# Optimization experiments

Hardware: AMD Instinct MI355X
Metric: run time of the kernel (lower is better)

The kernel has to match this reference:

```python
import jax, jax.numpy as jnp
import numpy as np

B, T, NH, HS = 2, 2048, 16, 64
C = NH * HS
V_SHIFT = 1          # value shift; queries start at position V_SHIFT
EXP_SCALE = 10.0     # exp_param_scale
KB_UP = 5.0          # kernel_beta_upbound


def setup_inputs() -> dict:
    key = jax.random.key(0)
    ks = jax.random.split(key, 8)
    s = 0.02
    return {
        "x": jax.random.normal(ks[0], (B, T, C), jnp.float32),
        # leaky-average key path: linear proj + per-head decay coefficient
        "W_la": jax.random.normal(ks[1], (C, C), jnp.float32) * s,
        "la_coef": jax.random.uniform(ks[2], (NH,), jnp.float32, 0.1, 0.9),
        "kernel_beta": jnp.ones((NH,), jnp.float32) / EXP_SCALE,
        "value_beta": jnp.ones((NH,), jnp.float32) * (-0.5) / EXP_SCALE,
        # value featurizer (lowrlinearconv): linear + per-head mixing coef
        "W_v": jax.random.normal(ks[3], (C, C), jnp.float32) * s,
        "v_coef": jax.random.uniform(ks[4], (NH,), jnp.float32, 0.0, 1.0),
        "W_proj": jax.random.normal(ks[5], (C, C), jnp.float32) * s,
    }


def reference(x, W_la, la_coef, kernel_beta, value_beta, W_v, v_coef, W_proj):
    B_, T_, C_ = x.shape
    # ---- keys: leaky average (per-head EMA recurrence) of linear projection ----
    xl = (x @ W_la).reshape(B_, T_, NH, HS)          # (B,T,nh,hs)
    alpha = la_coef.reshape(NH, 1)                   # per-head decay

    def step(carry, xt):  # carry,xt: (B,nh,hs)
        new = alpha * carry + (1.0 - alpha) * xt
        return new, new

    _, kt = jax.lax.scan(step, jnp.zeros((B_, NH, HS), x.dtype),
                         jnp.swapaxes(xl, 0, 1))    # (T,B,nh,hs)
    k = jnp.transpose(kt, (1, 2, 0, 3))              # (B,nh,T,hs)
    k = k / jnp.linalg.norm(k, axis=-1, keepdims=True)
    kb = jnp.exp(jnp.minimum(kernel_beta * EXP_SCALE, KB_UP)).reshape(1, NH, 1, 1)
    k = k * kb

    # ---- values: lowrlinearconv featurizer (shift=1, kernel=2) + L2 norm ----
    xv = (x @ W_v).reshape(B_, T_, NH, HS).transpose(0, 2, 1, 3)   # (B,nh,T,hs)
    xv_sh = jnp.concatenate([xv[:, :, 1:], jnp.zeros_like(xv[:, :, :1])], axis=2)
    c = v_coef.reshape(1, NH, 1, 1)
    v = xv_sh * (1.0 - c) + xv * c
    v = v / jnp.linalg.norm(v, axis=-1, keepdims=True)
    v = v * jnp.exp(value_beta * EXP_SCALE).reshape(1, NH, 1, 1)

    # ---- shifted-causal masked SDPA (scale=1); queries are positions >= V_SHIFT ----
    q = k[:, :, V_SHIFT:]                            # (B,nh,T-1,hs)
    scores = jnp.einsum('bhqd,bhkd->bhqk', q, k)
    qpos = jnp.arange(V_SHIFT, T_)[:, None]
    kpos = jnp.arange(T_)[None, :]
    mask = kpos < qpos                               # key j visible iff j < query position
    scores = jnp.where(mask, scores, -jnp.inf)
    att = jax.nn.softmax(scores, axis=-1)
    y_att = jnp.einsum('bhqk,bhkd->bhqd', att, v)
    y = jnp.concatenate([jnp.zeros((B_, NH, V_SHIFT, HS), x.dtype), y_att], axis=2)
    y = jnp.transpose(y, (0, 2, 1, 3)).reshape(B_, T_, C_)
    return y @ W_proj                                # dropouts are eval-mode identity
```

## Files before the change

kernel.cpp:

```cpp
#include <hip/hip_runtime.h>
#include <hip/hip_bf16.h>

#define B_  2
#define T_  2048
#define NH_ 16
#define HS_ 64
#define C_  1024
#define SCL_ 128
#define SCN_ (T_ / SCL_)
#define NT_  (T_ / 64)
#define TEL_ 4096

typedef __attribute__((ext_vector_type(8))) short bf16x8;
typedef __attribute__((ext_vector_type(4))) float f32x4;

__device__ inline int pack_bf16(float a, float b) {
  union { __hip_bfloat16 h; unsigned short u; } ua, ub;
  ua.h = __float2bfloat16(a);
  ub.h = __float2bfloat16(b);
  return (int)(((unsigned)ub.u << 16) | (unsigned)ua.u);
}

__device__ inline void gl_lds16(const __hip_bfloat16* g, __hip_bfloat16* l) {
  __builtin_amdgcn_global_load_lds(
      (const __attribute__((address_space(1))) unsigned int*)g,
      (__attribute__((address_space(3))) unsigned int*)l, 16, 0, 0);
}

__global__ __launch_bounds__(256) void cvt_bf16_kernel(const float* __restrict__ in,
                                                       __hip_bfloat16* __restrict__ out) {
  const int i = (blockIdx.x * 256 + threadIdx.x) * 8;
  const float4 a = *reinterpret_cast<const float4*>(in + i);
  const float4 b = *reinterpret_cast<const float4*>(in + i + 4);
  union { int s[4]; int4 v; } u;
  u.s[0] = pack_bf16(a.x, a.y);
  u.s[1] = pack_bf16(a.z, a.w);
  u.s[2] = pack_bf16(b.x, b.y);
  u.s[3] = pack_bf16(b.z, b.w);
  *reinterpret_cast<int4*>(out + i) = u.v;
}

__global__ __launch_bounds__(256) void cvtT_all_kernel(const float* __restrict__ W_la,
                                                       const float* __restrict__ W_v,
                                                       const float* __restrict__ W_proj,
                                                       __hip_bfloat16* __restrict__ Wcat,
                                                       __hip_bfloat16* __restrict__ WprojT) {
  __shared__ __hip_bfloat16 tile[64][66];
  const int z = blockIdx.z;
  const float* W = (z == 0) ? W_la : (z == 1) ? W_v : W_proj;
  __hip_bfloat16* WT = (z == 2) ? WprojT : Wcat + (size_t)z * C_ * C_;
  const int w = threadIdx.x >> 6, l = threadIdx.x & 63;
  const int n0 = blockIdx.x * 64, k0 = blockIdx.y * 64;
#pragma unroll
  for (int r = 0; r < 16; ++r) {
    const int k = k0 + w * 16 + r;
    tile[w * 16 + r][l] = __float2bfloat16(W[(size_t)k * C_ + n0 + l]);
  }
  __syncthreads();
#pragma unroll
  for (int r = 0; r < 16; ++r) {
    const int nn = w * 16 + r;
    WT[(size_t)(n0 + nn) * C_ + k0 + l] = tile[l][nn];
  }
}

__global__ __launch_bounds__(256) void gemm_in_kernel(const __hip_bfloat16* __restrict__ A,
                                                      const __hip_bfloat16* __restrict__ BT,
                                                      float* __restrict__ C0,
                                                      float* __restrict__ C1) {
  __shared__ __hip_bfloat16 As[2 * 128 * 32];
  __shared__ __hip_bfloat16 Bs[2 * 128 * 32];
  const int tid = threadIdx.x;
  const int m0 = blockIdx.y * 128, n0 = blockIdx.x * 128;
  const int w = tid >> 6, l = tid & 63;
  const int n = l & 15, kg = l >> 4;
  const int m0w = (w & 1) * 64, n0w = (w >> 1) * 64;

  const int r0 = tid >> 2, o0 = (tid & 3) * 8;
  const __hip_bfloat16* ag0 = A + (size_t)(m0 + r0) * C_ + o0;
  const __hip_bfloat16* ag1 = A + (size_t)(m0 + 64 + r0) * C_ + o0;
  const __hip_bfloat16* bg0 = BT + (size_t)(n0 + r0) * C_ + o0;
  const __hip_bfloat16* bg1 = BT + (size_t)(n0 + 64 + r0) * C_ + o0;

  f32x4 acc[4][4];
#pragma unroll
  for (int i = 0; i < 4; ++i)
#pragma unroll
    for (int j = 0; j < 4; ++j) acc[i][j] = f32x4{0.f, 0.f, 0.f, 0.f};

  auto stage = [&](int kk, int buf) {
    __hip_bfloat16* a = As + buf * 4096;
    __hip_bfloat16* b = Bs + buf * 4096;
    gl_lds16(ag0 + kk, a + tid * 8);
    gl_lds16(ag1 + kk, a + 2048 + tid * 8);
    gl_lds16(bg0 + kk, b + tid * 8);
    gl_lds16(bg1 + kk, b + 2048 + tid * 8);
  };

  stage(0, 0);
  int cur = 0;
  for (int k0 = 0; k0 < C_; k0 += 32) {
    asm volatile("" ::: "memory");
    __builtin_amdgcn_s_barrier();
    asm volatile("" ::: "memory");
    if (k0 + 32 < C_) {
      stage(k0 + 32, cur ^ 1);
      asm volatile("s_waitcnt vmcnt(4)" ::: "memory");
    } else {
      asm volatile("s_waitcnt vmcnt(0)" ::: "memory");
    }
    __builtin_amdgcn_s_barrier();
    asm volatile("" ::: "memory");

    const __hip_bfloat16* Ab = As + cur * 4096;
    const __hip_bfloat16* Bb = Bs + cur * 4096;
    bf16x8 af[4], bf[4];
#pragma unroll
    for (int ms = 0; ms < 4; ++ms)
      af[ms] = *reinterpret_cast<const bf16x8*>(Ab + (m0w + ms * 16 + n) * 32 + kg * 8);
#pragma unroll
    for (int ns = 0; ns < 4; ++ns)
      bf[ns] = *reinterpret_cast<const bf16x8*>(Bb + (n0w + ns * 16 + n) * 32 + kg * 8);
#pragma unroll
    for (int ms = 0; ms < 4; ++ms)
#pragma unroll
      for (int ns = 0; ns < 4; ++ns)
        acc[ms][ns] = __builtin_amdgcn_mfma_f32_16x16x32_bf16(af[ms], bf[ns], acc[ms][ns], 0, 0, 0);
    cur ^= 1;
  }

  float* Cb = (n0 < C_) ? C0 : C1;
  const int nc = (n0 < C_) ? n0 : n0 - C_;
#pragma unroll
  for (int ms = 0; ms < 4; ++ms) {
#pragma unroll
    for (int r = 0; r < 4; ++r) {
      const int row = m0 + m0w + ms * 16 + kg * 4 + r;
      float* cp = Cb + (size_t)row * C_ + nc + n0w + n;
#pragma unroll
      for (int ns = 0; ns < 4; ++ns) cp[ns * 16] = acc[ms][ns][r];
    }
  }
}

__global__ __launch_bounds__(256) void gemm_proj_kernel(const __hip_bfloat16* __restrict__ A,
                                                        const __hip_bfloat16* __restrict__ BT,
                                                        float* __restrict__ Cout) {
  __shared__ __hip_bfloat16 As[2 * 64 * 32];
  __shared__ __hip_bfloat16 Bs[2 * 128 * 32];
  const int tid = threadIdx.x;
  const int m0 = blockIdx.y * 64, n0 = blockIdx.x * 128;
  const int w = tid >> 6, l = tid & 63;
  const int n = l & 15, kg = l >> 4;

  const int r0 = tid >> 2, o0 = (tid & 3) * 8;
  const __hip_bfloat16* ag = A + (size_t)(m0 + r0) * C_ + o0;
  const __hip_bfloat16* bg0 = BT + (size_t)(n0 + r0) * C_ + o0;
  const __hip_bfloat16* bg1 = BT + (size_t)(n0 + 64 + r0) * C_ + o0;

  f32x4 acc[4][2];
#pragma unroll
  for (int i = 0; i < 4; ++i)
#pragma unroll
    for (int j = 0; j < 2; ++j) acc[i][j] = f32x4{0.f, 0.f, 0.f, 0.f};

  auto stage = [&](int kk, int buf) {
    __hip_bfloat16* a = As + buf * 2048;
    __hip_bfloat16* b = Bs + buf * 4096;
    gl_lds16(ag + kk, a + tid * 8);
    gl_lds16(bg0 + kk, b + tid * 8);
    gl_lds16(bg1 + kk, b + 2048 + tid * 8);
  };

  stage(0, 0);
  int cur = 0;
  for (int k0 = 0; k0 < C_; k0 += 32) {
    asm volatile("" ::: "memory");
    __builtin_amdgcn_s_barrier();
    asm volatile("" ::: "memory");
    if (k0 + 32 < C_) {
      stage(k0 + 32, cur ^ 1);
      asm volatile("s_waitcnt vmcnt(3)" ::: "memory");
    } else {
      asm volatile("s_waitcnt vmcnt(0)" ::: "memory");
    }
    __builtin_amdgcn_s_barrier();
    asm volatile("" ::: "memory");

    const __hip_bfloat16* Ab = As + cur * 2048;
    const __hip_bfloat16* Bb = Bs + cur * 4096;
    bf16x8 af[4], bf[2];
#pragma unroll
    for (int ms = 0; ms < 4; ++ms)
      af[ms] = *reinterpret_cast<const bf16x8*>(Ab + (ms * 16 + n) * 32 + kg * 8);
#pragma unroll
    for (int ns = 0; ns < 2; ++ns)
      bf[ns] = *reinterpret_cast<const bf16x8*>(Bb + (w * 32 + ns * 16 + n) * 32 + kg * 8);
#pragma unroll
    for (int ms = 0; ms < 4; ++ms)
#pragma unroll
      for (int ns = 0; ns < 2; ++ns)
        acc[ms][ns] = __builtin_amdgcn_mfma_f32_16x16x32_bf16(af[ms], bf[ns], acc[ms][ns], 0, 0, 0);
    cur ^= 1;
  }

#pragma unroll
  for (int ms = 0; ms < 4; ++ms) {
#pragma unroll
    for (int r = 0; r < 4; ++r) {
      const int row = m0 + ms * 16 + kg * 4 + r;
      float* cp = Cout + (size_t)row * C_ + n0 + w * 32 + n;
#pragma unroll
      for (int ns = 0; ns < 2; ++ns) cp[ns * 16] = acc[ms][ns][r];
    }
  }
}

__global__ __launch_bounds__(256) void ema_local_kernel(const float* __restrict__ xl,
                                                        float* __restrict__ loc,
                                                        float* __restrict__ carr,
                                                        const float* __restrict__ la_coef) {
  const int c = blockIdx.x % SCN_;
  const int bh = blockIdx.x / SCN_;
  const int b = bh / NH_, h = bh % NH_;
  const int tid = threadIdx.x;
  const int t0 = c * SCL_;
  __shared__ float buf[SCL_ * HS_];

  const float alpha = la_coef[h];
  const float onema = 1.0f - alpha;
  const float4* src4 = reinterpret_cast<const float4*>(xl + (size_t)b * T_ * C_ + h * HS_);

  float4* buf4 = reinterpret_cast<float4*>(buf);
#pragma unroll
  for (int i = 0; i < (SCL_ * HS_ / 4) / 256; ++i) {
    const int idx = tid + i * 256;
    const int tt = idx >> 4, d4 = idx & 15;
    buf4[tt * 16 + d4] = src4[(size_t)(t0 + tt) * (C_ / 4) + d4];
  }
  __syncthreads();
  if (tid < 64) {
    const int d = tid;
    float c2 = 0.0f;
#pragma unroll 8
    for (int tt = 0; tt < SCL_; ++tt) {
      c2 = alpha * c2 + onema * buf[tt * HS_ + d];
      buf[tt * HS_ + d] = c2;
    }
    carr[(size_t)(bh * SCN_ + c) * HS_ + d] = c2;
  }
  __syncthreads();
  float4* dst4 = reinterpret_cast<float4*>(loc + ((size_t)bh * T_ + t0) * HS_);
#pragma unroll
  for (int i = 0; i < (SCL_ * HS_ / 4) / 256; ++i) dst4[tid + i * 256] = buf4[tid + i * 256];
}

__global__ __launch_bounds__(256) void ema_fix_norm_kernel(const float* __restrict__ loc,
                                                           const float* __restrict__ carr,
                                                           __hip_bfloat16* __restrict__ kb16,
                                                           const float* __restrict__ la_coef,
                                                           const float* __restrict__ kernel_beta) {
  const int c = blockIdx.x % SCN_;
  const int bh = blockIdx.x / SCN_;
  const int h = bh % NH_;
  const int w = threadIdx.x >> 6, l = threadIdx.x & 63;

  const float alpha = la_coef[h];
  const float aL = __powf(alpha, (float)SCL_);
  const float kbs = expf(fminf(kernel_beta[h] * 10.0f, 5.0f));

  float A = 0.0f;
  for (int cc = 0; cc < c; ++cc) A = aL * A + carr[(size_t)(bh * SCN_ + cc) * HS_ + l];

  const float* lp = loc + ((size_t)bh * T_ + c * SCL_ + w * 32) * HS_ + l;
  __hip_bfloat16* kt = kb16 + (size_t)bh * NT_ * TEL_;
  const int g = l >> 3, j = l & 7;

  float s = __powf(alpha, (float)(w * 32 + 1));
  for (int rr = 0; rr < 32; ++rr) {
    const int t = c * SCL_ + w * 32 + rr;
    float val = lp[rr * HS_] + s * A;
    float ss = val * val;
#pragma unroll
    for (int m = 32; m; m >>= 1) ss += __shfl_xor(ss, m);
    const int tile = t >> 6, key = t & 63;
    kt[(size_t)tile * TEL_ + (g * 64 + key) * 8 + j] = __float2bfloat16(val * (kbs / sqrtf(ss)));
    s *= alpha;
  }
}

__global__ __launch_bounds__(256) void vprep_kernel(const float* __restrict__ xv,
                                                    __hip_bfloat16* __restrict__ vt,
                                                    const float* __restrict__ value_beta,
                                                    const float* __restrict__ v_coef) {
  const int tc = blockIdx.x % NT_;
  const int bh = blockIdx.x / NT_;
  const int h = bh % NH_, b = bh / NH_;
  const int t0 = tc * 64;
  const int w = threadIdx.x >> 6, l = threadIdx.x & 63;
  __shared__ __hip_bfloat16 tile[64][66];

  const float c = v_coef[h];
  const float vb = expf(value_beta[h] * 10.0f);

  for (int r = 0; r < 16; ++r) {
    const int tl = w * 16 + r;
    const int t = t0 + tl;
    const float* base = xv + ((size_t)b * T_ + t) * C_ + h * HS_ + l;
    const float cur = base[0];
    const float nxt = (t + 1 < T_) ? base[C_] : 0.0f;
    float val = nxt * (1.0f - c) + cur * c;
    float ssum = val * val;
#pragma unroll
    for (int m = 32; m; m >>= 1) ssum += __shfl_xor(ssum, m);
    tile[tl][l] = __float2bfloat16(val * (vb / sqrtf(ssum)));
  }
  __syncthreads();
  __hip_bfloat16* vtb = vt + (size_t)(bh * NT_ + tc) * TEL_;
  const int kk = l >> 3, j = l & 7;
  for (int rr = 0; rr < 16; ++rr) {
    const int hs = w * 16 + rr;
    vtb[(kk * 64 + hs) * 8 + j] = tile[l][hs];
  }
}

__global__ __launch_bounds__(256, 4) void attn_mfma_kernel(
    const __hip_bfloat16* __restrict__ kb,
    const __hip_bfloat16* __restrict__ vt,
    __hip_bfloat16* __restrict__ y) {
  __shared__ __hip_bfloat16 Ks[2 * TEL_];
  __shared__ __hip_bfloat16 Ps[4][16 * 64];

  const int id = (int)blockIdx.x;
  const int xcd = id & 7;
  const int s = id >> 3;
  const int bh = xcd + 8 * (s & 3);
  const int v = s >> 2;
  const int qt = (v < 16) ? (31 - v) : (v - 16);
  const int b = bh / NH_, h = bh % NH_;
  const int q0 = qt * 64;
  const int w = threadIdx.x >> 6;
  const int l = threadIdx.x & 63;
  const int n = l & 15;
  const int kg = l >> 4;
  const int qq = w * 16 + n;
  const int query = q0 + qq;
  const int lo = l * 8;
  const int tb = bh * NT_;
  const int so = w * 1024 + lo;

  bf16x8 qf0, qf1;
  {
    const __hip_bfloat16* qtile = kb + (size_t)(tb + qt) * TEL_;
    qf0 = *reinterpret_cast<const bf16x8*>(qtile + (kg * 64 + qq) * 8);
    qf1 = *reinterpret_cast<const bf16x8*>(qtile + ((kg + 4) * 64 + qq) * 8);
  }
  const __hip_bfloat16* vbase = vt + (size_t)tb * TEL_ + (kg * 64 + n) * 8;

  f32x4 accO[4];
#pragma unroll
  for (int i = 0; i < 4; ++i) accO[i] = f32x4{0.f, 0.f, 0.f, 0.f};
  float l_acc = 0.0f;

  __hip_bfloat16* Pw = Ps[w];
  int* Pwi = reinterpret_cast<int*>(Pw);

  {
    const size_t tg = (size_t)tb * TEL_;
    gl_lds16(kb + tg + so, Ks + so);
    gl_lds16(kb + tg + so + 512, Ks + so + 512);
  }

  int cur = 0;
  for (int jt = 0; jt <= qt; ++jt) {
    asm volatile("" ::: "memory");
    __builtin_amdgcn_s_barrier();
    asm volatile("" ::: "memory");

    bf16x8 vf[2][4];
    {
      const __hip_bfloat16* vp = vbase + (size_t)jt * TEL_;
#pragma unroll
      for (int ks = 0; ks < 2; ++ks)
#pragma unroll
        for (int mo = 0; mo < 4; ++mo)
          vf[ks][mo] = *reinterpret_cast<const bf16x8*>(vp + ks * 2048 + mo * 128);
    }
    asm volatile("" ::: "memory");

    if (jt < qt) {
      const size_t tg = (size_t)(tb + jt + 1) * TEL_;
      const int bo = (cur ^ 1) * TEL_ + so;
      gl_lds16(kb + tg + so, Ks + bo);
      gl_lds16(kb + tg + so + 512, Ks + bo + 512);
      asm volatile("s_waitcnt vmcnt(10)" ::: "memory");
    } else {
      asm volatile("s_waitcnt vmcnt(8)" ::: "memory");
    }
    __builtin_amdgcn_s_barrier();
    asm volatile("" ::: "memory");

    const __hip_bfloat16* Kc = Ks + cur * TEL_;

    f32x4 accS[4];
    __builtin_amdgcn_s_setprio(1);
#pragma unroll
    for (int ms = 0; ms < 4; ++ms) {
      bf16x8 a0 = *reinterpret_cast<const bf16x8*>(Kc + (kg * 64 + ms * 16 + n) * 8);
      bf16x8 a1 = *reinterpret_cast<const bf16x8*>(Kc + ((kg + 4) * 64 + ms * 16 + n) * 8);
      f32x4 z{0.f, 0.f, 0.f, 0.f};
      z = __builtin_amdgcn_mfma_f32_16x16x32_bf16(a0, qf0, z, 0, 0, 0);
      accS[ms] = __builtin_amdgcn_mfma_f32_16x16x32_bf16(a1, qf1, z, 0, 0, 0);
    }
    __builtin_amdgcn_s_setprio(0);

    if (jt < qt) {
#pragma unroll
      for (int ms = 0; ms < 4; ++ms) {
        float p[4];
#pragma unroll
        for (int r = 0; r < 4; ++r) {
          p[r] = __expf(accS[ms][r]);
          l_acc += p[r];
        }
        const int po = n * 32 + (((ms * 4 + kg) ^ n) << 1);
        int2 pw;
        pw.x = pack_bf16(p[0], p[1]);
        pw.y = pack_bf16(p[2], p[3]);
        *reinterpret_cast<int2*>(&Pwi[po]) = pw;
      }
    } else {
#pragma unroll
      for (int ms = 0; ms < 4; ++ms) {
        const int kbase = ms * 16 + kg * 4;
        float p[4];
#pragma unroll
        for (int r = 0; r < 4; ++r) {
          const float e = __expf(accS[ms][r]);
          p[r] = (kbase + r < qq) ? e : 0.0f;
          l_acc += p[r];
        }
        const int po = n * 32 + (((ms * 4 + kg) ^ n) << 1);
        int2 pw;
        pw.x = pack_bf16(p[0], p[1]);
        pw.y = pack_bf16(p[2], p[3]);
        *reinterpret_cast<int2*>(&Pwi[po]) = pw;
      }
    }

    __builtin_amdgcn_s_setprio(1);
#pragma unroll
    for (int ks = 0; ks < 2; ++ks) {
      union { ushort4 u[2]; bf16x8 v; } pr;
      const int ga = (ks * 8 + kg * 2) ^ n;
      const __hip_bfloat16* pp = Pw + n * 64;
      pr.u[0] = *reinterpret_cast<const ushort4*>(pp + ga * 4);
      pr.u[1] = *reinterpret_cast<const ushort4*>(pp + (ga ^ 1) * 4);
#pragma unroll
      for (int mo = 0; mo < 4; ++mo)
        accO[mo] = __builtin_amdgcn_mfma_f32_16x16x32_bf16(vf[ks][mo], pr.v, accO[mo], 0, 0, 0);
    }
    __builtin_amdgcn_s_setprio(0);

    cur ^= 1;
  }

  l_acc += __shfl_xor(l_acc, 16);
  l_acc += __shfl_xor(l_acc, 32);
  const float inv = (query == 0) ? 0.0f : 1.0f / l_acc;
  __hip_bfloat16* yb = y + ((size_t)b * T_ + query) * C_ + h * HS_;
#pragma unroll
  for (int mo = 0; mo < 4; ++mo) {
    int2 pkd;
    pkd.x = pack_bf16(accO[mo][0] * inv, accO[mo][1] * inv);
    pkd.y = pack_bf16(accO[mo][2] * inv, accO[mo][3] * inv);
    *reinterpret_cast<int2*>(yb + mo * 16 + kg * 4) = pkd;
  }
}

extern "C" void kernel_launch(void* const* d_in, const int* in_sizes, int n_in,
                              void* d_out, int out_size, void* d_ws, size_t ws_size,
                              hipStream_t stream) {
  const float* x           = (const float*)d_in[0];
  const float* W_la        = (const float*)d_in[1];
  const float* la_coef     = (const float*)d_in[2];
  const float* kernel_beta = (const float*)d_in[3];
  const float* value_beta  = (const float*)d_in[4];
  const float* W_v         = (const float*)d_in[5];
  const float* v_coef      = (const float*)d_in[6];
  const float* W_proj      = (const float*)d_in[7];
  float* out = (float*)d_out;

  char* wsb = (char*)d_ws;
  const size_t MB = 1024u * 1024u;
  __hip_bfloat16* x16    = (__hip_bfloat16*)(wsb);
  __hip_bfloat16* Wcat   = (__hip_bfloat16*)(wsb + 8 * MB);
  __hip_bfloat16* WprojT = (__hip_bfloat16*)(wsb + 12 * MB);
  float* carr            = (float*)(wsb + 14 * MB);
  float* xl              = (float*)(wsb + 16 * MB);
  float* xv              = (float*)(wsb + 32 * MB);
  __hip_bfloat16* kb16   = (__hip_bfloat16*)(wsb + 48 * MB);
  __hip_bfloat16* vt16   = (__hip_bfloat16*)(wsb + 56 * MB);
  float* loc             = xv;
  __hip_bfloat16* y16    = (__hip_bfloat16*)(wsb + 16 * MB);
  (void)ws_size; (void)in_sizes; (void)n_in; (void)out_size;

  const int M = B_ * T_;

  cvt_bf16_kernel<<<dim3((M * C_) / 2048), dim3(256), 0, stream>>>(x, x16);
  cvtT_all_kernel<<<dim3(C_ / 64, C_ / 64, 3), dim3(256), 0, stream>>>(W_la, W_v, W_proj, Wcat, WprojT);

  gemm_in_kernel<<<dim3(2 * C_ / 128, M / 128), dim3(256), 0, stream>>>(x16, Wcat, xl, xv);
  vprep_kernel<<<dim3(B_ * NH_ * NT_), dim3(256), 0, stream>>>(xv, vt16, value_beta, v_coef);
  ema_local_kernel<<<dim3(B_ * NH_ * SCN_), dim3(256), 0, stream>>>(xl, loc, carr, la_coef);
  ema_fix_norm_kernel<<<dim3(B_ * NH_ * SCN_), dim3(256), 0, stream>>>(loc, carr, kb16, la_coef, kernel_beta);
  attn_mfma_kernel<<<dim3(8 * 128), dim3(256), 0, stream>>>(kb16, vt16, y16);
  gemm_proj_kernel<<<dim3(C_ / 128, M / 64), dim3(256), 0, stream>>>(y16, WprojT, out);
}
```

Before: 218.6 us.

## Merge prep kernels and stage two key tiles per attention iteration

Merges the x and weight conversion kernels into one launch, and the value-prep and local-EMA kernels into another. Because these now run concurrently, the EMA output moves to its own workspace buffer instead of aliasing xv. The attention loop now loads two 64-key tiles per barrier pair into a larger double buffer, halving the barriers and waits per key range. This trades launch and sync overhead for more LDS per block, which may lower occupancy.

```diff
diff --git a/kernel.cpp b/kernel.cpp
--- a/kernel.cpp
+++ b/kernel.cpp
@@ -27,30 +27,35 @@
       (__attribute__((address_space(3))) unsigned int*)l, 16, 0, 0);
 }
 
-__global__ __launch_bounds__(256) void cvt_bf16_kernel(const float* __restrict__ in,
-                                                       __hip_bfloat16* __restrict__ out) {
-  const int i = (blockIdx.x * 256 + threadIdx.x) * 8;
-  const float4 a = *reinterpret_cast<const float4*>(in + i);
-  const float4 b = *reinterpret_cast<const float4*>(in + i + 4);
-  union { int s[4]; int4 v; } u;
-  u.s[0] = pack_bf16(a.x, a.y);
-  u.s[1] = pack_bf16(a.z, a.w);
-  u.s[2] = pack_bf16(b.x, b.y);
-  u.s[3] = pack_bf16(b.z, b.w);
-  *reinterpret_cast<int4*>(out + i) = u.v;
-}
-
-__global__ __launch_bounds__(256) void cvtT_all_kernel(const float* __restrict__ W_la,
-                                                       const float* __restrict__ W_v,
-                                                       const float* __restrict__ W_proj,
-                                                       __hip_bfloat16* __restrict__ Wcat,
-                                                       __hip_bfloat16* __restrict__ WprojT) {
+__global__ __launch_bounds__(256) void prep1_kernel(const float* __restrict__ x,
+                                                    const float* __restrict__ W_la,
+                                                    const float* __restrict__ W_v,
+                                                    const float* __restrict__ W_proj,
+                                                    __hip_bfloat16* __restrict__ x16,
+                                                    __hip_bfloat16* __restrict__ Wcat,
+                                                    __hip_bfloat16* __restrict__ WprojT) {
   __shared__ __hip_bfloat16 tile[64][66];
-  const int z = blockIdx.z;
+  const int bid = (int)blockIdx.x;
+  if (bid < 2048) {
+    const int i = (bid * 256 + (int)threadIdx.x) * 8;
+    const float4 a = *reinterpret_cast<const float4*>(x + i);
+    const float4 b = *reinterpret_cast<const float4*>(x + i + 4);
+    union { int s[4]; int4 v; } u;
+    u.s[0] = pack_bf16(a.x, a.y);
+    u.s[1] = pack_bf16(a.z, a.w);
+    u.s[2] = pack_bf16(b.x, b.y);
+    u.s[3] = pack_bf16(b.z, b.w);
+    *reinterpret_cast<int4*>(x16 + i) = u.v;
+    return;
+  }
+  const int id = bid - 2048;
+  const int z = id >> 8;
+  const int rem = id & 255;
+  const int bx = rem & 15, by = rem >> 4;
   const float* W = (z == 0) ? W_la : (z == 1) ? W_v : W_proj;
   __hip_bfloat16* WT = (z == 2) ? WprojT : Wcat + (size_t)z * C_ * C_;
   const int w = threadIdx.x >> 6, l = threadIdx.x & 63;
-  const int n0 = blockIdx.x * 64, k0 = blockIdx.y * 64;
+  const int n0 = bx * 64, k0 = by * 64;
 #pragma unroll
   for (int r = 0; r < 16; ++r) {
     const int k = k0 + w * 16 + r;
@@ -216,43 +221,84 @@
   }
 }
 
-__global__ __launch_bounds__(256) void ema_local_kernel(const float* __restrict__ xl,
-                                                        float* __restrict__ loc,
-                                                        float* __restrict__ carr,
-                                                        const float* __restrict__ la_coef) {
-  const int c = blockIdx.x % SCN_;
-  const int bh = blockIdx.x / SCN_;
-  const int b = bh / NH_, h = bh % NH_;
-  const int tid = threadIdx.x;
-  const int t0 = c * SCL_;
-  __shared__ float buf[SCL_ * HS_];
-
-  const float alpha = la_coef[h];
-  const float onema = 1.0f - alpha;
-  const float4* src4 = reinterpret_cast<const float4*>(xl + (size_t)b * T_ * C_ + h * HS_);
-
-  float4* buf4 = reinterpret_cast<float4*>(buf);
-#pragma unroll
-  for (int i = 0; i < (SCL_ * HS_ / 4) / 256; ++i) {
-    const int idx = tid + i * 256;
-    const int tt = idx >> 4, d4 = idx & 15;
-    buf4[tt * 16 + d4] = src4[(size_t)(t0 + tt) * (C_ / 4) + d4];
-  }
-  __syncthreads();
-  if (tid < 64) {
-    const int d = tid;
-    float c2 = 0.0f;
+__global__ __launch_bounds__(256) void prep2_kernel(const float* __restrict__ xv,
+                                                    const float* __restrict__ xl,
+                                                    __hip_bfloat16* __restrict__ vt,
+                                                    float* __restrict__ loc,
+                                                    float* __restrict__ carr,
+                                                    const float* __restrict__ value_beta,
+                                                    const float* __restrict__ v_coef,
+                                                    const float* __restrict__ la_coef) {
+  __shared__ float4 smem4[2048];
+  const int bid = (int)blockIdx.x;
+  if (bid < 1024) {
+    __hip_bfloat16 (*tile)[66] = reinterpret_cast<__hip_bfloat16(*)[66]>(smem4);
+    const int tc = bid % NT_;
+    const int bh = bid / NT_;
+    const int h = bh % NH_, b = bh / NH_;
+    const int t0 = tc * 64;
+    const int w = threadIdx.x >> 6, l = threadIdx.x & 63;
+
+    const float c = v_coef[h];
+    const float vb = expf(value_beta[h] * 10.0f);
+
+    for (int r = 0; r < 16; ++r) {
+      const int tl = w * 16 + r;
+      const int t = t0 + tl;
+      const float* base = xv + ((size_t)b * T_ + t) * C_ + h * HS_ + l;
+      const float cu = base[0];
+      const float nxt = (t + 1 < T_) ? base[C_] : 0.0f;
+      float val = nxt * (1.0f - c) + cu * c;
+      float ssum = val * val;
+#pragma unroll
+      for (int m = 32; m; m >>= 1) ssum += __shfl_xor(ssum, m);
+      tile[tl][l] = __float2bfloat16(val * (vb / sqrtf(ssum)));
+    }
+    __syncthreads();
+    __hip_bfloat16* vtb = vt + (size_t)(bh * NT_ + tc) * TEL_;
+    const int kk = l >> 3, j = l & 7;
+    for (int rr = 0; rr < 16; ++rr) {
+      const int hs = w * 16 + rr;
+      vtb[(kk * 64 + hs) * 8 + j] = tile[l][hs];
+    }
+    return;
+  }
+  {
+    float* buf = reinterpret_cast<float*>(smem4);
+    const int idx = bid - 1024;
+    const int c = idx % SCN_;
+    const int bh = idx / SCN_;
+    const int b = bh / NH_, h = bh % NH_;
+    const int tid = threadIdx.x;
+    const int t0 = c * SCL_;
+
+    const float alpha = la_coef[h];
+    const float onema = 1.0f - alpha;
+    const float4* src4 = reinterpret_cast<const float4*>(xl + (size_t)b * T_ * C_ + h * HS_);
+
+    float4* buf4 = reinterpret_cast<float4*>(buf);
+#pragma unroll
+    for (int i = 0; i < (SCL_ * HS_ / 4) / 256; ++i) {
+      const int ix = tid + i * 256;
+      const int tt = ix >> 4, d4 = ix & 15;
+      buf4[tt * 16 + d4] = src4[(size_t)(t0 + tt) * (C_ / 4) + d4];
+    }
+    __syncthreads();
+    if (tid < 64) {
+      const int d = tid;
+      float c2 = 0.0f;
 #pragma unroll 8
-    for (int tt = 0; tt < SCL_; ++tt) {
-      c2 = alpha * c2 + onema * buf[tt * HS_ + d];
-      buf[tt * HS_ + d] = c2;
-    }
-    carr[(size_t)(bh * SCN_ + c) * HS_ + d] = c2;
-  }
-  __syncthreads();
-  float4* dst4 = reinterpret_cast<float4*>(loc + ((size_t)bh * T_ + t0) * HS_);
-#pragma unroll
-  for (int i = 0; i < (SCL_ * HS_ / 4) / 256; ++i) dst4[tid + i * 256] = buf4[tid + i * 256];
+      for (int tt = 0; tt < SCL_; ++tt) {
+        c2 = alpha * c2 + onema * buf[tt * HS_ + d];
+        buf[tt * HS_ + d] = c2;
+      }
+      carr[(size_t)(bh * SCN_ + c) * HS_ + d] = c2;
+    }
+    __syncthreads();
+    float4* dst4 = reinterpret_cast<float4*>(loc + ((size_t)bh * T_ + t0) * HS_);
+#pragma unroll
+    for (int i = 0; i < (SCL_ * HS_ / 4) / 256; ++i) dst4[tid + i * 256] = buf4[tid + i * 256];
+  }
 }
 
 __global__ __launch_bounds__(256) void ema_fix_norm_kernel(const float* __restrict__ loc,
@@ -289,46 +335,11 @@
   }
 }
 
-__global__ __launch_bounds__(256) void vprep_kernel(const float* __restrict__ xv,
-                                                    __hip_bfloat16* __restrict__ vt,
-                                                    const float* __restrict__ value_beta,
-                                                    const float* __restrict__ v_coef) {
-  const int tc = blockIdx.x % NT_;
-  const int bh = blockIdx.x / NT_;
-  const int h = bh % NH_, b = bh / NH_;
-  const int t0 = tc * 64;
-  const int w = threadIdx.x >> 6, l = threadIdx.x & 63;
-  __shared__ __hip_bfloat16 tile[64][66];
-
-  const float c = v_coef[h];
-  const float vb = expf(value_beta[h] * 10.0f);
-
-  for (int r = 0; r < 16; ++r) {
-    const int tl = w * 16 + r;
-    const int t = t0 + tl;
-    const float* base = xv + ((size_t)b * T_ + t) * C_ + h * HS_ + l;
-    const float cur = base[0];
-    const float nxt = (t + 1 < T_) ? base[C_] : 0.0f;
-    float val = nxt * (1.0f - c) + cur * c;
-    float ssum = val * val;
-#pragma unroll
-    for (int m = 32; m; m >>= 1) ssum += __shfl_xor(ssum, m);
-    tile[tl][l] = __float2bfloat16(val * (vb / sqrtf(ssum)));
-  }
-  __syncthreads();
-  __hip_bfloat16* vtb = vt + (size_t)(bh * NT_ + tc) * TEL_;
-  const int kk = l >> 3, j = l & 7;
-  for (int rr = 0; rr < 16; ++rr) {
-    const int hs = w * 16 + rr;
-    vtb[(kk * 64 + hs) * 8 + j] = tile[l][hs];
-  }
-}
-
 __global__ __launch_bounds__(256, 4) void attn_mfma_kernel(
     const __hip_bfloat16* __restrict__ kb,
     const __hip_bfloat16* __restrict__ vt,
     __hip_bfloat16* __restrict__ y) {
-  __shared__ __hip_bfloat16 Ks[2 * TEL_];
+  __shared__ __hip_bfloat16 Ks[2][2 * TEL_];
   __shared__ __hip_bfloat16 Ps[4][16 * 64];
 
   const int id = (int)blockIdx.x;
@@ -365,44 +376,29 @@
   __hip_bfloat16* Pw = Ps[w];
   int* Pwi = reinterpret_cast<int*>(Pw);
 
-  {
-    const size_t tg = (size_t)tb * TEL_;
-    gl_lds16(kb + tg + so, Ks + so);
-    gl_lds16(kb + tg + so + 512, Ks + so + 512);
-  }
-
-  int cur = 0;
-  for (int jt = 0; jt <= qt; ++jt) {
-    asm volatile("" ::: "memory");
-    __builtin_amdgcn_s_barrier();
-    asm volatile("" ::: "memory");
-
-    bf16x8 vf[2][4];
-    {
-      const __hip_bfloat16* vp = vbase + (size_t)jt * TEL_;
-#pragma unroll
-      for (int ks = 0; ks < 2; ++ks)
-#pragma unroll
-        for (int mo = 0; mo < 4; ++mo)
-          vf[ks][mo] = *reinterpret_cast<const bf16x8*>(vp + ks * 2048 + mo * 128);
-    }
-    asm volatile("" ::: "memory");
-
-    if (jt < qt) {
-      const size_t tg = (size_t)(tb + jt + 1) * TEL_;
-      const int bo = (cur ^ 1) * TEL_ + so;
-      gl_lds16(kb + tg + so, Ks + bo);
-      gl_lds16(kb + tg + so + 512, Ks + bo + 512);
-      asm volatile("s_waitcnt vmcnt(10)" ::: "memory");
-    } else {
-      asm volatile("s_waitcnt vmcnt(8)" ::: "memory");
-    }
-    __builtin_amdgcn_s_barrier();
-    asm volatile("" ::: "memory");
-
-    const __hip_bfloat16* Kc = Ks + cur * TEL_;
-
-    f32x4 accS[4];
+  auto stage2 = [&](int j0, int buf) {
+    const size_t tg = (size_t)(tb + j0) * TEL_;
+    __hip_bfloat16* Kb = &Ks[buf][0];
+    gl_lds16(kb + tg + so, Kb + so);
+    gl_lds16(kb + tg + so + 512, Kb + so + 512);
+    gl_lds16(kb + tg + TEL_ + so, Kb + TEL_ + so);
+    gl_lds16(kb + tg + TEL_ + so + 512, Kb + TEL_ + so + 512);
+  };
+  auto stage1 = [&](int j0, int buf) {
+    const size_t tg = (size_t)(tb + j0) * TEL_;
+    __hip_bfloat16* Kb = &Ks[buf][0];
+    gl_lds16(kb + tg + so, Kb + so);
+    gl_lds16(kb + tg + so + 512, Kb + so + 512);
+  };
+  auto loadV = [&](int jt, bf16x8 (&vf)[2][4]) {
+    const __hip_bfloat16* vp = vbase + (size_t)jt * TEL_;
+#pragma unroll
+    for (int ks = 0; ks < 2; ++ks)
+#pragma unroll
+      for (int mo = 0; mo < 4; ++mo)
+        vf[ks][mo] = *reinterpret_cast<const bf16x8*>(vp + ks * 2048 + mo * 128);
+  };
+  auto computeS = [&](const __hip_bfloat16* Kc, f32x4 (&accS)[4]) {
     __builtin_amdgcn_s_setprio(1);
 #pragma unroll
     for (int ms = 0; ms < 4; ++ms) {
@@ -413,20 +409,18 @@
       accS[ms] = __builtin_amdgcn_mfma_f32_16x16x32_bf16(a1, qf1, z, 0, 0, 0);
     }
     __builtin_amdgcn_s_setprio(0);
-
-    if (jt < qt) {
+  };
+  auto softmaxStore = [&](const f32x4 (&accS)[4], bool diag) {
+    if (!diag) {
 #pragma unroll
       for (int ms = 0; ms < 4; ++ms) {
-        float p[4];
-#pragma unroll
-        for (int r = 0; r < 4; ++r) {
-          p[r] = __expf(accS[ms][r]);
-          l_acc += p[r];
-        }
+        const float p0 = __expf(accS[ms][0]), p1 = __expf(accS[ms][1]);
+        const float p2 = __expf(accS[ms][2]), p3 = __expf(accS[ms][3]);
+        l_acc += p0 + p1 + p2 + p3;
         const int po = n * 32 + (((ms * 4 + kg) ^ n) << 1);
         int2 pw;
-        pw.x = pack_bf16(p[0], p[1]);
-        pw.y = pack_bf16(p[2], p[3]);
+        pw.x = pack_bf16(p0, p1);
+        pw.y = pack_bf16(p2, p3);
         *reinterpret_cast<int2*>(&Pwi[po]) = pw;
       }
     } else {
@@ -447,22 +441,77 @@
         *reinterpret_cast<int2*>(&Pwi[po]) = pw;
       }
     }
-
+  };
+  auto pv = [&](const bf16x8 (&vf)[2][4]) {
     __builtin_amdgcn_s_setprio(1);
 #pragma unroll
     for (int ks = 0; ks < 2; ++ks) {
-      union { ushort4 u[2]; bf16x8 v; } pr;
+      union { ushort4 u[2]; bf16x8 vv; } pr;
       const int ga = (ks * 8 + kg * 2) ^ n;
       const __hip_bfloat16* pp = Pw + n * 64;
       pr.u[0] = *reinterpret_cast<const ushort4*>(pp + ga * 4);
       pr.u[1] = *reinterpret_cast<const ushort4*>(pp + (ga ^ 1) * 4);
 #pragma unroll
       for (int mo = 0; mo < 4; ++mo)
-        accO[mo] = __builtin_amdgcn_mfma_f32_16x16x32_bf16(vf[ks][mo], pr.v, accO[mo], 0, 0, 0);
+        accO[mo] = __builtin_amdgcn_mfma_f32_16x16x32_bf16(vf[ks][mo], pr.vv, accO[mo], 0, 0, 0);
     }
     __builtin_amdgcn_s_setprio(0);
+  };
+
+  if (qt >= 1) stage2(0, 0); else stage1(0, 0);
+
+  int cur = 0;
+  int jp = 0;
+  for (; jp + 1 <= qt; jp += 2) {
+    asm volatile("" ::: "memory");
+    __builtin_amdgcn_s_barrier();
+    asm volatile("" ::: "memory");
+
+    bf16x8 vfA[2][4];
+    loadV(jp, vfA);
+    asm volatile("" ::: "memory");
+
+    const int nx = jp + 2;
+    if (nx + 1 <= qt) {
+      stage2(nx, cur ^ 1);
+      asm volatile("s_waitcnt vmcnt(12)" ::: "memory");
+    } else if (nx <= qt) {
+      stage1(nx, cur ^ 1);
+      asm volatile("s_waitcnt vmcnt(10)" ::: "memory");
+    } else {
+      asm volatile("s_waitcnt vmcnt(8)" ::: "memory");
+    }
+    __builtin_amdgcn_s_barrier();
+    asm volatile("" ::: "memory");
+
+    f32x4 accS[4];
+    computeS(&Ks[cur][0], accS);
+    softmaxStore(accS, false);
+    pv(vfA);
+
+    asm volatile("" ::: "memory");
+
+    bf16x8 vfB[2][4];
+    loadV(jp + 1, vfB);
+    computeS(&Ks[cur][TEL_], accS);
+    softmaxStore(accS, jp + 1 == qt);
+    pv(vfB);
 
     cur ^= 1;
+  }
+  if (jp <= qt) {
+    asm volatile("" ::: "memory");
+    __builtin_amdgcn_s_barrier();
+    asm volatile("" ::: "memory");
+    bf16x8 vfA[2][4];
+    loadV(jp, vfA);
+    asm volatile("s_waitcnt vmcnt(8)" ::: "memory");
+    __builtin_amdgcn_s_barrier();
+    asm volatile("" ::: "memory");
+    f32x4 accS[4];
+    computeS(&Ks[cur][0], accS);
+    softmaxStore(accS, true);
+    pv(vfA);
   }
 
   l_acc += __shfl_xor(l_acc, 16);
@@ -501,18 +550,16 @@
   float* xv              = (float*)(wsb + 32 * MB);
   __hip_bfloat16* kb16   = (__hip_bfloat16*)(wsb + 48 * MB);
   __hip_bfloat16* vt16   = (__hip_bfloat16*)(wsb + 56 * MB);
-  float* loc             = xv;
+  float* loc             = (float*)(wsb + 64 * MB);
   __hip_bfloat16* y16    = (__hip_bfloat16*)(wsb + 16 * MB);
   (void)ws_size; (void)in_sizes; (void)n_in; (void)out_size;
 
   const int M = B_ * T_;
 
-  cvt_bf16_kernel<<<dim3((M * C_) / 2048), dim3(256), 0, stream>>>(x, x16);
-  cvtT_all_kernel<<<dim3(C_ / 64, C_ / 64, 3), dim3(256), 0, stream>>>(W_la, W_v, W_proj, Wcat, WprojT);
-
+  prep1_kernel<<<dim3(2048 + 768), dim3(256), 0, stream>>>(x, W_la, W_v, W_proj, x16, Wcat, WprojT);
   gemm_in_kernel<<<dim3(2 * C_ / 128, M / 128), dim3(256), 0, stream>>>(x16, Wcat, xl, xv);
-  vprep_kernel<<<dim3(B_ * NH_ * NT_), dim3(256), 0, stream>>>(xv, vt16, value_beta, v_coef);
-  ema_local_kernel<<<dim3(B_ * NH_ * SCN_), dim3(256), 0, stream>>>(xl, loc, carr, la_coef);
+  prep2_kernel<<<dim3(1024 + 512), dim3(256), 0, stream>>>(xv, xl, vt16, loc, carr,
+                                                           value_beta, v_coef, la_coef);
   ema_fix_norm_kernel<<<dim3(B_ * NH_ * SCN_), dim3(256), 0, stream>>>(loc, carr, kb16, la_coef, kernel_beta);
   attn_mfma_kernel<<<dim3(8 * 128), dim3(256), 0, stream>>>(kb16, vt16, y16);
   gemm_proj_kernel<<<dim3(C_ / 128, M / 64), dim3(256), 0, stream>>>(y16, WprojT, out);
```

New measurement: 203.2 us. 1.08x faster.
